# Optimization experiments

Hardware: AMD Instinct MI355X
Metric: run time of the kernel (lower is better)

## Reference

```python
import jax, jax.numpy as jnp
import numpy as np

B, H, S, D = 1, 16, 2048, 64


def setup_inputs() -> dict:
    key = jax.random.key(0)
    kq, kk, kv, km = jax.random.split(key, 4)
    q = jax.random.normal(kq, (B, H, S, D), dtype=jnp.float32)
    k = jax.random.normal(kk, (B, H, S, D), dtype=jnp.float32)
    v = jax.random.normal(kv, (B, H, S, D), dtype=jnp.float32)
    omask = jax.random.uniform(km, (B, H, S, S), dtype=jnp.float32)
    return {"q": q, "k": k, "v": v, "omask": omask}


def reference(q, k, v, omask):
    # mask = omask / sqrt(rowsum(omask)), nan -> 0
    row_sum = jnp.sum(omask, axis=-1, keepdims=True)  # [B,H,S,1]
    decay_mask = jnp.nan_to_num(omask / jnp.sqrt(row_sum), nan=0.0)
    # retention = (q k^T) * mask  -> [B,H,S,S]
    retention = jnp.einsum("bhsd,bhtd->bhst", q, k) * decay_mask
    # normalize by |rowsum(retention)| clamped to >= 1 (detached in original)
    scale = jnp.clip(jnp.abs(jnp.sum(retention, axis=-1, keepdims=True)), 1.0, None)
    retention = retention / scale
    # output = retention @ v -> [B,H,S,D]
    return jnp.einsum("bhst,bhtd->bhsd", retention, v)
```

## Files before the change

### kernel.cpp

```cpp
#include <hip/hip_runtime.h>

#define H 16
#define S 2048
#define D 64
#define BM 64
#define BN 64
#define KP 72

typedef __attribute__((ext_vector_type(8))) short bf16x8;
typedef __attribute__((ext_vector_type(4))) short short4v;
typedef __attribute__((ext_vector_type(4))) float fx4;

static __device__ __forceinline__ short f2bf(float x) {
    unsigned u = __float_as_uint(x);
    u += 0x7fffu + ((u >> 16) & 1u);
    return (short)(u >> 16);
}
static __device__ __forceinline__ float bf2f(short s) {
    return __uint_as_float(((unsigned)(unsigned short)s) << 16);
}

__global__ __launch_bounds__(256)
void ParallelRetention_origin_25374666785438_kernel(
    const float* __restrict__ q, const float* __restrict__ k,
    const float* __restrict__ v, const float* __restrict__ om,
    float* __restrict__ out)
{
    __shared__ short ldsKh[BN * KP];
    __shared__ short ldsKl[BN * KP];
    __shared__ short ldsVT[D * KP];
    __shared__ short ldsP[4 * 16 * KP];

    const int tid  = threadIdx.x;
    const int wave = tid >> 6;
    const int lane = tid & 63;
    const int col  = lane & 15;
    const int quad = lane >> 4;

    const int h  = blockIdx.x & 15;
    const int qb = blockIdx.x >> 4;
    const int row0 = qb * BM;

    const size_t headQK = (size_t)h * S * D;
    const size_t headM  = (size_t)h * S * S;

    bf16x8 qh[2], ql[2];
    {
        const int s_row = row0 + wave * 16 + col;
        const float* qp = q + headQK + (size_t)s_row * D + quad * 8;
#pragma unroll
        for (int c = 0; c < 2; ++c) {
            fx4 a = *(const fx4*)(qp + c * 32);
            fx4 b = *(const fx4*)(qp + c * 32 + 4);
            float f[8] = {a[0],a[1],a[2],a[3],b[0],b[1],b[2],b[3]};
#pragma unroll
            for (int j = 0; j < 8; ++j) {
                short hi = f2bf(f[j]);
                qh[c][j] = hi;
                ql[c][j] = f2bf(f[j] - bf2f(hi));
            }
        }
    }

    fx4 U[4];
#pragma unroll
    for (int nt = 0; nt < 4; ++nt) { U[nt][0]=0.f; U[nt][1]=0.f; U[nt][2]=0.f; U[nt][3]=0.f; }
    float rs_acc[4] = {0.f, 0.f, 0.f, 0.f};
    float T_acc[4]  = {0.f, 0.f, 0.f, 0.f};

    const float* kbase0 = k + headQK;
    const float* vbase0 = v + headQK;
    const float* ombase = om + headM + (size_t)(row0 + wave * 16) * S;

    for (int t0 = 0; t0 < S; t0 += BN) {
        __syncthreads();
        {
            const float* kb = kbase0 + (size_t)t0 * D;
            const float* vb = vbase0 + (size_t)t0 * D;
#pragma unroll
            for (int i = 0; i < 4; ++i) {
                int g  = tid + i * 256;
                int t  = g >> 4;
                int d4 = (g & 15) << 2;
                fx4 kv = *(const fx4*)(kb + (size_t)t * D + d4);
                fx4 vv = *(const fx4*)(vb + (size_t)t * D + d4);
                short4v k4h, k4l;
#pragma unroll
                for (int j = 0; j < 4; ++j) {
                    short hi = f2bf(kv[j]);
                    k4h[j] = hi;
                    k4l[j] = f2bf(kv[j] - bf2f(hi));
                }
                *(short4v*)(&ldsKh[t * KP + d4]) = k4h;
                *(short4v*)(&ldsKl[t * KP + d4]) = k4l;
                ldsVT[(d4 + 0) * KP + t] = f2bf(vv[0]);
                ldsVT[(d4 + 1) * KP + t] = f2bf(vv[1]);
                ldsVT[(d4 + 2) * KP + t] = f2bf(vv[2]);
                ldsVT[(d4 + 3) * KP + t] = f2bf(vv[3]);
            }
        }
        __syncthreads();

        fx4 Sc[4];
#pragma unroll
        for (int tn = 0; tn < 4; ++tn) {
            const short* kph = &ldsKh[(tn * 16 + col) * KP + quad * 8];
            const short* kpl = &ldsKl[(tn * 16 + col) * KP + quad * 8];
            bf16x8 kh0 = *(const bf16x8*)(kph);
            bf16x8 kh1 = *(const bf16x8*)(kph + 32);
            bf16x8 kl0 = *(const bf16x8*)(kpl);
            bf16x8 kl1 = *(const bf16x8*)(kpl + 32);
            fx4 z; z[0]=0.f; z[1]=0.f; z[2]=0.f; z[3]=0.f;
            z = __builtin_amdgcn_mfma_f32_16x16x32_bf16(qh[0], kh0, z, 0, 0, 0);
            z = __builtin_amdgcn_mfma_f32_16x16x32_bf16(qh[1], kh1, z, 0, 0, 0);
            z = __builtin_amdgcn_mfma_f32_16x16x32_bf16(qh[0], kl0, z, 0, 0, 0);
            z = __builtin_amdgcn_mfma_f32_16x16x32_bf16(qh[1], kl1, z, 0, 0, 0);
            z = __builtin_amdgcn_mfma_f32_16x16x32_bf16(ql[0], kh0, z, 0, 0, 0);
            z = __builtin_amdgcn_mfma_f32_16x16x32_bf16(ql[1], kh1, z, 0, 0, 0);
            Sc[tn] = z;
        }

        const float* omp = ombase + t0;
        float omv[4][4];
#pragma unroll
        for (int tn = 0; tn < 4; ++tn)
#pragma unroll
            for (int r = 0; r < 4; ++r)
                omv[tn][r] = omp[(size_t)(quad * 4 + r) * S + tn * 16 + col];

#pragma unroll
        for (int tn = 0; tn < 4; ++tn) {
#pragma unroll
            for (int r = 0; r < 4; ++r) {
                float m = omv[tn][r];
                float p = Sc[tn][r] * m;
                rs_acc[r] += m;
                T_acc[r]  += p;
                ldsP[(wave * 16 + quad * 4 + r) * KP + tn * 16 + col] = f2bf(p);
            }
        }

#pragma unroll
        for (int kt = 0; kt < 2; ++kt) {
            bf16x8 pa = *(const bf16x8*)(&ldsP[(wave * 16 + col) * KP + kt * 32 + quad * 8]);
#pragma unroll
            for (int nt = 0; nt < 4; ++nt) {
                bf16x8 vb = *(const bf16x8*)(&ldsVT[(nt * 16 + col) * KP + kt * 32 + quad * 8]);
                U[nt] = __builtin_amdgcn_mfma_f32_16x16x32_bf16(pa, vb, U[nt], 0, 0, 0);
            }
        }
    }

#pragma unroll
    for (int off = 1; off < 16; off <<= 1) {
#pragma unroll
        for (int r = 0; r < 4; ++r) {
            rs_acc[r] += __shfl_xor(rs_acc[r], off, 64);
            T_acc[r]  += __shfl_xor(T_acc[r], off, 64);
        }
    }
    float factor[4];
#pragma unroll
    for (int r = 0; r < 4; ++r) {
        float rs  = rs_acc[r];
        float inv = rs > 0.f ? rsqrtf(rs) : 0.f;
        float rowsum = T_acc[r] * inv;
        float sc = fabsf(rowsum);
        sc = sc < 1.f ? 1.f : sc;
        factor[r] = inv / sc;
    }
    float* op = out + headQK + (size_t)(row0 + wave * 16) * D;
#pragma unroll
    for (int r = 0; r < 4; ++r)
#pragma unroll
        for (int nt = 0; nt < 4; ++nt)
            op[(size_t)(quad * 4 + r) * D + nt * 16 + col] = U[nt][r] * factor[r];
}

extern "C" void kernel_launch(void* const* d_in, const int* in_sizes, int n_in,
                              void* d_out, int out_size, void* d_ws, size_t ws_size,
                              hipStream_t stream) {
    const float* q  = (const float*)d_in[0];
    const float* k  = (const float*)d_in[1];
    const float* v  = (const float*)d_in[2];
    const float* om = (const float*)d_in[3];
    float* out = (float*)d_out;
    (void)in_sizes; (void)n_in; (void)out_size; (void)d_ws; (void)ws_size;

    dim3 grid(H * (S / BM));
    dim3 block(256);
    hipLaunchKernelGGL(ParallelRetention_origin_25374666785438_kernel,
                       grid, block, 0, stream, q, k, v, om, out);
}
```

Baseline: 470.0 us.

## Double-buffer K/V tiles in LDS and prefetch next tile and omask into registers

Splits the K/V LDS staging into two buffers. The next tile's K, V and omask values are loaded into registers before computing on the current tile, then converted and written to the other buffer afterward. This hides global-memory latency behind the MFMA work and cuts the loop to one barrier per tile. It also remaps thread-to-element assignment so V-transpose LDS writes become 4-wide vector stores instead of scalar stores. The cost is more LDS and higher register pressure, which may reduce occupancy.

```diff
diff --git a/kernel.cpp b/kernel.cpp
--- a/kernel.cpp
+++ b/kernel.cpp
@@ -5,6 +5,7 @@
 #define D 64
 #define BM 64
 #define BN 64
+#define NT (S / BN)
 #define KP 72
 
 typedef __attribute__((ext_vector_type(8))) short bf16x8;
@@ -26,9 +27,9 @@
     const float* __restrict__ v, const float* __restrict__ om,
     float* __restrict__ out)
 {
-    __shared__ short ldsKh[BN * KP];
-    __shared__ short ldsKl[BN * KP];
-    __shared__ short ldsVT[D * KP];
+    __shared__ short ldsKh[2][BN * KP];
+    __shared__ short ldsKl[2][BN * KP];
+    __shared__ short ldsVT[2][BN * KP];
     __shared__ short ldsP[4 * 16 * KP];
 
     const int tid  = threadIdx.x;
@@ -36,6 +37,8 @@
     const int lane = tid & 63;
     const int col  = lane & 15;
     const int quad = lane >> 4;
+    const int t_base = (tid >> 4) << 2;
+    const int d4     = (tid & 15) << 2;
 
     const int h  = blockIdx.x & 15;
     const int qb = blockIdx.x >> 4;
@@ -44,7 +47,7 @@
     const size_t headQK = (size_t)h * S * D;
     const size_t headM  = (size_t)h * S * S;
 
-    bf16x8 qh[2], ql[2];
+    bf16x8 qh[2], qlo[2];
     {
         const int s_row = row0 + wave * 16 + col;
         const float* qp = q + headQK + (size_t)s_row * D + quad * 8;
@@ -56,8 +59,8 @@
 #pragma unroll
             for (int j = 0; j < 8; ++j) {
                 short hi = f2bf(f[j]);
-                qh[c][j] = hi;
-                ql[c][j] = f2bf(f[j] - bf2f(hi));
+                qh[c][j]  = hi;
+                qlo[c][j] = f2bf(f[j] - bf2f(hi));
             }
         }
     }
@@ -67,87 +70,114 @@
     for (int nt = 0; nt < 4; ++nt) { U[nt][0]=0.f; U[nt][1]=0.f; U[nt][2]=0.f; U[nt][3]=0.f; }
     float rs_acc[4] = {0.f, 0.f, 0.f, 0.f};
     float T_acc[4]  = {0.f, 0.f, 0.f, 0.f};
+    float om0[16], om1[16];
 
     const float* kbase0 = k + headQK;
     const float* vbase0 = v + headQK;
     const float* ombase = om + headM + (size_t)(row0 + wave * 16) * S;
 
-    for (int t0 = 0; t0 < S; t0 += BN) {
-        __syncthreads();
-        {
-            const float* kb = kbase0 + (size_t)t0 * D;
-            const float* vb = vbase0 + (size_t)t0 * D;
-#pragma unroll
-            for (int i = 0; i < 4; ++i) {
-                int g  = tid + i * 256;
-                int t  = g >> 4;
-                int d4 = (g & 15) << 2;
-                fx4 kv = *(const fx4*)(kb + (size_t)t * D + d4);
-                fx4 vv = *(const fx4*)(vb + (size_t)t * D + d4);
-                short4v k4h, k4l;
-#pragma unroll
-                for (int j = 0; j < 4; ++j) {
-                    short hi = f2bf(kv[j]);
-                    k4h[j] = hi;
-                    k4l[j] = f2bf(kv[j] - bf2f(hi));
-                }
-                *(short4v*)(&ldsKh[t * KP + d4]) = k4h;
-                *(short4v*)(&ldsKl[t * KP + d4]) = k4l;
-                ldsVT[(d4 + 0) * KP + t] = f2bf(vv[0]);
-                ldsVT[(d4 + 1) * KP + t] = f2bf(vv[1]);
-                ldsVT[(d4 + 2) * KP + t] = f2bf(vv[2]);
-                ldsVT[(d4 + 3) * KP + t] = f2bf(vv[3]);
-            }
-        }
-        __syncthreads();
-
-        fx4 Sc[4];
+    auto load_kv = [&](int t0, fx4 (&kr)[4], fx4 (&vr)[4]) {
+        const float* kb = kbase0 + (size_t)t0 * D;
+        const float* vb = vbase0 + (size_t)t0 * D;
+#pragma unroll
+        for (int r = 0; r < 4; ++r) {
+            kr[r] = *(const fx4*)(kb + (size_t)(t_base + r) * D + d4);
+            vr[r] = *(const fx4*)(vb + (size_t)(t_base + r) * D + d4);
+        }
+    };
+    auto load_om = [&](int t0, float (&o)[16]) {
+        const float* omp = ombase + t0;
+#pragma unroll
+        for (int tn = 0; tn < 4; ++tn)
+#pragma unroll
+            for (int r = 0; r < 4; ++r)
+                o[tn * 4 + r] = omp[(size_t)(quad * 4 + r) * S + tn * 16 + col];
+    };
+    auto stage_write = [&](const fx4 (&kr)[4], const fx4 (&vr)[4],
+                           short* Kh, short* Kl, short* VT) {
+#pragma unroll
+        for (int r = 0; r < 4; ++r) {
+            short4v h4, l4;
+#pragma unroll
+            for (int j = 0; j < 4; ++j) {
+                short hi = f2bf(kr[r][j]);
+                h4[j] = hi;
+                l4[j] = f2bf(kr[r][j] - bf2f(hi));
+            }
+            *(short4v*)(&Kh[(t_base + r) * KP + d4]) = h4;
+            *(short4v*)(&Kl[(t_base + r) * KP + d4]) = l4;
+        }
+#pragma unroll
+        for (int j = 0; j < 4; ++j) {
+            short4v p;
+#pragma unroll
+            for (int r = 0; r < 4; ++r) p[r] = f2bf(vr[r][j]);
+            *(short4v*)(&VT[(d4 + j) * KP + t_base]) = p;
+        }
+    };
+    auto compute = [&](const short* Kh, const short* Kl, const short* VT,
+                       const float (&omc)[16]) {
 #pragma unroll
         for (int tn = 0; tn < 4; ++tn) {
-            const short* kph = &ldsKh[(tn * 16 + col) * KP + quad * 8];
-            const short* kpl = &ldsKl[(tn * 16 + col) * KP + quad * 8];
+            const short* kph = &Kh[(tn * 16 + col) * KP + quad * 8];
+            const short* kpl = &Kl[(tn * 16 + col) * KP + quad * 8];
             bf16x8 kh0 = *(const bf16x8*)(kph);
             bf16x8 kh1 = *(const bf16x8*)(kph + 32);
             bf16x8 kl0 = *(const bf16x8*)(kpl);
             bf16x8 kl1 = *(const bf16x8*)(kpl + 32);
             fx4 z; z[0]=0.f; z[1]=0.f; z[2]=0.f; z[3]=0.f;
-            z = __builtin_amdgcn_mfma_f32_16x16x32_bf16(qh[0], kh0, z, 0, 0, 0);
-            z = __builtin_amdgcn_mfma_f32_16x16x32_bf16(qh[1], kh1, z, 0, 0, 0);
-            z = __builtin_amdgcn_mfma_f32_16x16x32_bf16(qh[0], kl0, z, 0, 0, 0);
-            z = __builtin_amdgcn_mfma_f32_16x16x32_bf16(qh[1], kl1, z, 0, 0, 0);
-            z = __builtin_amdgcn_mfma_f32_16x16x32_bf16(ql[0], kh0, z, 0, 0, 0);
-            z = __builtin_amdgcn_mfma_f32_16x16x32_bf16(ql[1], kh1, z, 0, 0, 0);
-            Sc[tn] = z;
-        }
-
-        const float* omp = ombase + t0;
-        float omv[4][4];
-#pragma unroll
-        for (int tn = 0; tn < 4; ++tn)
-#pragma unroll
-            for (int r = 0; r < 4; ++r)
-                omv[tn][r] = omp[(size_t)(quad * 4 + r) * S + tn * 16 + col];
-
-#pragma unroll
-        for (int tn = 0; tn < 4; ++tn) {
+            z = __builtin_amdgcn_mfma_f32_16x16x32_bf16(qh[0],  kh0, z, 0, 0, 0);
+            z = __builtin_amdgcn_mfma_f32_16x16x32_bf16(qh[1],  kh1, z, 0, 0, 0);
+            z = __builtin_amdgcn_mfma_f32_16x16x32_bf16(qh[0],  kl0, z, 0, 0, 0);
+            z = __builtin_amdgcn_mfma_f32_16x16x32_bf16(qh[1],  kl1, z, 0, 0, 0);
+            z = __builtin_amdgcn_mfma_f32_16x16x32_bf16(qlo[0], kh0, z, 0, 0, 0);
+            z = __builtin_amdgcn_mfma_f32_16x16x32_bf16(qlo[1], kh1, z, 0, 0, 0);
 #pragma unroll
             for (int r = 0; r < 4; ++r) {
-                float m = omv[tn][r];
-                float p = Sc[tn][r] * m;
+                float m = omc[tn * 4 + r];
+                float p = z[r] * m;
                 rs_acc[r] += m;
                 T_acc[r]  += p;
                 ldsP[(wave * 16 + quad * 4 + r) * KP + tn * 16 + col] = f2bf(p);
             }
         }
-
 #pragma unroll
         for (int kt = 0; kt < 2; ++kt) {
             bf16x8 pa = *(const bf16x8*)(&ldsP[(wave * 16 + col) * KP + kt * 32 + quad * 8]);
 #pragma unroll
             for (int nt = 0; nt < 4; ++nt) {
-                bf16x8 vb = *(const bf16x8*)(&ldsVT[(nt * 16 + col) * KP + kt * 32 + quad * 8]);
+                bf16x8 vb = *(const bf16x8*)(&VT[(nt * 16 + col) * KP + kt * 32 + quad * 8]);
                 U[nt] = __builtin_amdgcn_mfma_f32_16x16x32_bf16(pa, vb, U[nt], 0, 0, 0);
             }
+        }
+    };
+
+    {
+        fx4 kr[4], vr[4];
+        load_kv(0, kr, vr);
+        load_om(0, om0);
+        stage_write(kr, vr, ldsKh[0], ldsKl[0], ldsVT[0]);
+    }
+
+    for (int it2 = 0; it2 < NT; it2 += 2) {
+        {
+            __syncthreads();
+            fx4 kr[4], vr[4];
+            load_kv((it2 + 1) * BN, kr, vr);
+            load_om((it2 + 1) * BN, om1);
+            compute(ldsKh[0], ldsKl[0], ldsVT[0], om0);
+            stage_write(kr, vr, ldsKh[1], ldsKl[1], ldsVT[1]);
+        }
+        {
+            __syncthreads();
+            const bool pf = (it2 + 2 < NT);
+            fx4 kr[4], vr[4];
+            if (pf) {
+                load_kv((it2 + 2) * BN, kr, vr);
+                load_om((it2 + 2) * BN, om0);
+            }
+            compute(ldsKh[1], ldsKl[1], ldsVT[1], om1);
+            if (pf) stage_write(kr, vr, ldsKh[0], ldsKl[0], ldsVT[0]);
         }
     }
 
```

Result: faster. 407.1 us (-13.4%).
